# Performance work log

Hardware: AMD Instinct MI355X
Metric: run time of the kernel (lower is better)

The kernel has to match this reference:

```python
import jax, jax.numpy as jnp
import numpy as np

N = 65536          # nodes
G = 512            # graphs (num_segments for scatter-mean)
NB = 10            # number_of_basis
MAXR = 10.0        # max_radius
NODE_DIM = 64      # 48 z-embed + 16 mol-embed scalars
MUL = 16           # multiplicity of each output irrep l=0..3
WNUM = NODE_DIM * 4 * MUL  # tp weight numel = 4096
MID = 32           # middle_layer_size

_trapz = getattr(np, 'trapezoid', np.trapz)

def _silu_norm():
    # e3nn normalize2mom constant for silu: 1/sqrt(E_{z~N(0,1)}[silu(z)^2]) ~= 1.679
    z = np.linspace(-12.0, 12.0, 200001)
    pdf = np.exp(-0.5 * z * z) / np.sqrt(2.0 * np.pi)
    s = z / (1.0 + np.exp(-z))
    return float(_trapz(s * s * pdf, z) ** -0.5)

SILU_C = _silu_norm()

def soft_unit_step(x):
    pos = x > 0
    return jnp.where(pos, jnp.exp(-1.0 / jnp.where(pos, x, 1.0)), 0.0)

def soft_one_hot_smooth_finite(x):
    # e3nn soft_one_hot_linspace(basis='smooth_finite', cutoff=True)
    values = jnp.linspace(0.0, MAXR, NB + 2)[1:-1]
    step = MAXR / (NB + 1)
    diff = (x[:, None] - values) / step
    c = 1.14136 * float(np.exp(2.0))
    return c * soft_unit_step(diff + 1.0) * soft_unit_step(1.0 - diff)

def spherical_harmonics_lmax3(vec):
    # e3nn convention, normalize=True, normalization='component' (each l scaled by sqrt(2l+1))
    u = vec / jnp.linalg.norm(vec, axis=-1, keepdims=True)
    x, y, z = u[..., 0], u[..., 1], u[..., 2]
    s3 = np.sqrt(3.0)
    y2, x2z2 = y * y, x * x + z * z
    sh0 = jnp.ones_like(x)[..., None]
    s20 = s3 * x * z; s21 = s3 * x * y; s22 = y2 - 0.5 * x2z2
    s23 = s3 * y * z; s24 = 0.5 * s3 * (z * z - x * x)
    s30 = np.sqrt(5.0 / 6.0) * (s20 * z + s24 * x)
    s31 = np.sqrt(5.0) * s20 * y
    s32 = np.sqrt(3.0 / 8.0) * (4.0 * y2 - x2z2) * x
    s33 = 0.5 * y * (2.0 * y2 - 3.0 * x2z2)
    s34 = np.sqrt(3.0 / 8.0) * z * (4.0 * y2 - x2z2)
    s35 = np.sqrt(5.0) * s24 * y
    s36 = np.sqrt(5.0 / 6.0) * (s24 * z - s20 * x)
    sh1 = np.sqrt(3.0) * jnp.stack([x, y, z], -1)
    sh2 = np.sqrt(5.0) * jnp.stack([s20, s21, s22, s23, s24], -1)
    sh3 = np.sqrt(7.0) * jnp.stack([s30, s31, s32, s33, s34, s35, s36], -1)
    return (sh0, sh1, sh2, sh3)

def setup_inputs() -> dict:
    key = jax.random.key(0)
    ks = jax.random.split(key, 8)
    pos = 3.0 * jax.random.normal(ks[0], (N, 3), jnp.float32)
    x = jax.random.randint(ks[1], (N,), 0, 100)
    mol_id = jax.random.randint(ks[2], (N,), 0, 3)
    batch = jnp.sort(jax.random.randint(ks[3], (N,), 0, G))
    emb_z = jax.random.normal(ks[4], (100, 48), jnp.float32)
    emb_mol = jax.random.normal(ks[5], (3, 16), jnp.float32)
    W1 = jax.random.normal(ks[6], (NB, MID), jnp.float32)
    W2 = jax.random.normal(ks[7], (MID, WNUM), jnp.float32)
    return {'pos': pos, 'x': x, 'mol_id': mol_id, 'batch': batch,
            'emb_z': emb_z, 'emb_mol': emb_mol, 'W1': W1, 'W2': W2}

def reference(pos, x, mol_id, batch, emb_z, emb_mol, W1, W2):
    feat = jnp.concatenate([emb_z[x], emb_mol[mol_id]], axis=-1)        # [N, 64]
    length = jnp.linalg.norm(pos, axis=1)
    basis = soft_one_hot_smooth_finite(length) * np.sqrt(float(NB))     # [N, 10]
    # e3nn FullyConnectedNet([10, 32, 4096], silu): weight / sqrt(fan_in), normalized silu
    h = SILU_C * jax.nn.silu(basis @ (W1 / np.sqrt(float(NB))))         # [N, 32]
    w = h @ (W2 / np.sqrt(float(MID)))                                  # [N, 4096]
    # path weight sqrt((2l+1)/64) times w3j(0,l,l)=I/sqrt(2l+1) -> net factor 1/sqrt(64)
    w = w.reshape(-1, 4, NODE_DIM, MUL)
    xw = jnp.einsum('eu,eluw->elw', feat, w) / np.sqrt(float(NODE_DIM))  # [N, 4, 16]
    shs = spherical_harmonics_lmax3(pos)
    blocks = [(xw[:, l, :, None] * shs[l][:, None, :]).reshape(-1, MUL * (2 * l + 1)) for l in range(4)]
    value = jnp.concatenate(blocks, axis=-1)                            # [N, 256]
    sums = jax.ops.segment_sum(value, batch, num_segments=G)
    counts = jax.ops.segment_sum(jnp.ones((value.shape[0], 1), value.dtype), batch, num_segments=G)
    return sums / jnp.maximum(counts, 1.0)                              # scatter-mean [G, 256]
```

## Files before the change

kernel.cpp:

```cpp
#include <hip/hip_runtime.h>
#include <math.h>

#define N_NODES 65536
#define G_SEG   512
#define NE      256

#define NB_HS 33
#define NB_Q  128
#define NB_QM 32
#define NB_S  3
#define NB_P0 (N_NODES / 256)
#define NB_K1 (NB_HS + NB_Q + NB_QM + NB_S + NB_P0)

#define NB_A  1700
#define NB_B2 257
#define NB_K2 (NB_A + NB_B2)

#define A_ELEMS  (257 * 100 * 64)
#define B_ELEMS  (257 * 3 * 64)
#define Q_ELEMS  (100 * 32 * 64)
#define QM_ELEMS (3 * 32 * 64)
#define HS_ELEMS (257 * 32)

__global__ __launch_bounds__(256) void prep1(
    const float* __restrict__ emb_z, const float* __restrict__ emb_mol,
    const float* __restrict__ W2, const float* __restrict__ W1,
    const int* __restrict__ batch,
    const float* __restrict__ pos, const int* __restrict__ xz,
    const int* __restrict__ mol,
    float* __restrict__ Q, float* __restrict__ Qm, float* __restrict__ hs,
    int* __restrict__ seg, float4* __restrict__ aux, float silu_c)
{
    __shared__ float w2s[64 * 49];
    __shared__ float ezq[1200];

    const int b = blockIdx.x;
    const int t = threadIdx.x;

    if (b < NB_HS) {
        const int tid = b * 256 + t;
        if (tid >= HS_ELEMS) return;
        const int e = tid >> 5, m = tid & 31;
        const float L = (float)e * (10.f / (float)NE);
        const float c = 8.4335412f;
        float p = 0.f;
#pragma unroll
        for (int k = 0; k < 10; ++k) {
            const float a  = 1.1f * L - (float)k;
            const float bb = (float)(k + 2) - 1.1f * L;
            const float bas = (a > 0.f && bb > 0.f) ? c * __expf(-2.f / (a * bb)) : 0.f;
            p = fmaf(bas, W1[k * 32 + m], p);
        }
        const float scale = 0.02209708691207961f;
        hs[tid] = scale * silu_c * p / (1.f + __expf(-p));
    } else if (b < NB_HS + NB_Q) {
        const int q  = b - NB_HS;
        const int m  = q >> 2;
        const int zq = q & 3;
        for (int p = t; p < 3072; p += 256) {
            const int l = p / 768, r = p - l * 768;
            w2s[((l * 16) + (r & 15)) * 49 + (r >> 4)] = W2[m * 4096 + l * 1024 + r];
        }
        for (int p = t; p < 1200; p += 256) ezq[p] = emb_z[zq * 1200 + p];
        __syncthreads();

        const int zg = t >> 6, cc = t & 63;
#pragma unroll
        for (int zi = 0; zi < 7; ++zi) {
            const int zl = zg + 4 * zi;
            if (zl < 25) {
                float a0 = 0.f, a1 = 0.f, a2 = 0.f, a3 = 0.f;
#pragma unroll
                for (int u = 0; u < 48; u += 4) {
                    a0 = fmaf(ezq[zl * 48 + u + 0], w2s[cc * 49 + u + 0], a0);
                    a1 = fmaf(ezq[zl * 48 + u + 1], w2s[cc * 49 + u + 1], a1);
                    a2 = fmaf(ezq[zl * 48 + u + 2], w2s[cc * 49 + u + 2], a2);
                    a3 = fmaf(ezq[zl * 48 + u + 3], w2s[cc * 49 + u + 3], a3);
                }
                Q[(((zq * 25 + zl) * 32 + m) << 6) + cc] = (a0 + a1) + (a2 + a3);
            }
        }
    } else if (b < NB_HS + NB_Q + NB_QM) {
        const int m = b - (NB_HS + NB_Q);
        if (t < 192) {
            const int mo = t >> 6, j = t & 63;
            const float* wp = W2 + m * 4096 + (j >> 4) * 1024 + 768 + (j & 15);
            float acc = 0.f;
#pragma unroll
            for (int v = 0; v < 16; ++v)
                acc = fmaf(emb_mol[mo * 16 + v], wp[v * 16], acc);
            Qm[((mo * 32 + m) << 6) + j] = acc;
        }
    } else if (b < NB_HS + NB_Q + NB_QM + NB_S) {
        const int g = (b - NB_HS - NB_Q - NB_QM) * 256 + t;
        if (g > G_SEG) return;
        int lo = 0, hi = N_NODES;
        while (lo < hi) {
            const int mid = (lo + hi) >> 1;
            if (batch[mid] < g) lo = mid + 1; else hi = mid;
        }
        seg[g] = lo;
    } else {
        const int i = (b - NB_HS - NB_Q - NB_QM - NB_S) * 256 + t;
        const float px = pos[3 * i], py = pos[3 * i + 1], pz = pos[3 * i + 2];
        const int z  = xz[i];
        const int mo = mol[i];
        const float Lsq = px * px + py * py + pz * pz;
        const float rinv = __builtin_amdgcn_rsqf(Lsq);
        const float L = Lsq * rinv;
        const float tt = fminf(L * ((float)NE / 10.0f), 255.999f);
        const int e = (int)tt;
        const int fr15 = min((int)((tt - (float)e) * 32768.f), 32767);
        float4 a;
        a.x = px * rinv; a.y = py * rinv; a.z = pz * rinv;
        a.w = __uint_as_float(((unsigned)e << 24) | ((unsigned)z << 17) |
                              ((unsigned)mo << 15) | (unsigned)fr15);
        aux[i] = a;
    }
}

__global__ __launch_bounds__(256) void build_AB2(
    const float* __restrict__ Q, const float* __restrict__ Qm,
    const float* __restrict__ hs,
    float* __restrict__ A, float* __restrict__ B)
{
    const int b = blockIdx.x;
    const int t = threadIdx.x;
    const int j = t & 63;
    const int er = __builtin_amdgcn_readfirstlane(t >> 6);

    if (b < NB_A) {
        const int et = b / 100;
        const int z  = b - et * 100;
        float Qr[32];
        const float* Qp = Q + ((z * 32) << 6) + j;
#pragma unroll
        for (int m = 0; m < 32; ++m) Qr[m] = Qp[m << 6];

        const int e0 = et * 16;
#pragma unroll
        for (int p4 = 0; p4 < 4; ++p4) {
            const int e = e0 + er + 4 * p4;
            if (e < 257) {
                const float* hp = hs + e * 32;
                float a0 = 0.f, a1 = 0.f, a2 = 0.f, a3 = 0.f;
#pragma unroll
                for (int m = 0; m < 32; m += 4) {
                    a0 = fmaf(hp[m + 0], Qr[m + 0], a0);
                    a1 = fmaf(hp[m + 1], Qr[m + 1], a1);
                    a2 = fmaf(hp[m + 2], Qr[m + 2], a2);
                    a3 = fmaf(hp[m + 3], Qr[m + 3], a3);
                }
                A[((e * 100 + z) << 6) + j] = (a0 + a1) + (a2 + a3);
            }
        }
    } else {
        const int e  = b - NB_A;
        const int mo = t >> 6;
        if (mo < 3) {
            const float* Qp = Qm + ((mo * 32) << 6) + j;
            const float* hp = hs + e * 32;
            float acc = 0.f;
#pragma unroll
            for (int m = 0; m < 32; ++m)
                acc = fmaf(hp[m], Qp[m << 6], acc);
            B[((e * 3 + mo) << 6) + j] = acc;
        }
    }
}

__global__ __launch_bounds__(1024) void seg_mean(
    const float4* __restrict__ aux, const int* __restrict__ seg,
    const float* __restrict__ A, const float* __restrict__ B,
    float* __restrict__ out)
{
    __shared__ float red[16 * 257];

    const int g  = blockIdx.x;
    const int s0 = seg[g], s1 = seg[g + 1];
    const int cnt = s1 - s0;

    const int w16  = __builtin_amdgcn_readfirstlane(threadIdx.x >> 6);
    const int l    = w16 & 3;
    const int qt   = w16 >> 2;
    const int lane = threadIdx.x & 63;
    const int ns   = lane >> 4;
    const int wi   = lane & 15;
    const int jj   = l * 16 + wi;

    const int q0 = s0 + ((cnt * qt) >> 2);
    const int q1 = s0 + ((cnt * (qt + 1)) >> 2);

    float acc[7];
#pragma unroll
    for (int k = 0; k < 7; ++k) acc[k] = 0.f;

    const int niter = (q1 - q0 + 3) >> 2;

    float4 aN = make_float4(0.f, 0.f, 1.f, __uint_as_float(0u));
    float a0N = 0.f, a1N = 0.f, b0N = 0.f, b1N = 0.f;
    if (niter > 0) {
        const int ic = min(q0 + ns, q1 - 1);
        aN = aux[ic];
        const unsigned cd = __float_as_uint(aN.w);
        const float* Ar = A + (((cd >> 24) * 100 + ((cd >> 17) & 127u)) << 6) + jj;
        const float* Br = B + (((cd >> 24) * 3 + ((cd >> 15) & 3u)) << 6) + jj;
        a0N = Ar[0]; a1N = Ar[6400]; b0N = Br[0]; b1N = Br[192];
    }

    for (int it = 0; it < niter; ++it) {
        const float4 a = aN;
        const float f0 = a0N + b0N, f1 = a1N + b1N;
        const unsigned code = __float_as_uint(a.w);
        const int i = q0 + it * 4 + ns;
        const bool valid = (i < q1);

        if (it + 1 < niter) {
            const int ic = min(q0 + (it + 1) * 4 + ns, q1 - 1);
            aN = aux[ic];
            const unsigned cn = __float_as_uint(aN.w);
            const float* Ar = A + (((cn >> 24) * 100 + ((cn >> 17) & 127u)) << 6) + jj;
            const float* Br = B + (((cn >> 24) * 3 + ((cn >> 15) & 3u)) << 6) + jj;
            a0N = Ar[0]; a1N = Ar[6400]; b0N = Br[0]; b1N = Br[192];
        }

        const float fr = (float)(code & 32767u) * 3.0517578125e-5f;
        float xwv = fmaf(fr, f1 - f0, f0);
        xwv = valid ? xwv : 0.f;

        const float ux = a.x, uy = a.y, uz = a.z;
        const float s3 = 1.7320508075688772f, s5 = 2.2360679774997896f, s7 = 2.6457513110645907f;

        if (l == 0) {
            acc[0] += xwv;
        } else if (l == 1) {
            acc[0] = fmaf(xwv, s3 * ux, acc[0]);
            acc[1] = fmaf(xwv, s3 * uy, acc[1]);
            acc[2] = fmaf(xwv, s3 * uz, acc[2]);
        } else if (l == 2) {
            const float y2 = uy * uy, x2z2 = ux * ux + uz * uz;
            const float s20 = s3 * ux * uz;
            const float s21 = s3 * ux * uy;
            const float s22 = y2 - 0.5f * x2z2;
            const float s23 = s3 * uy * uz;
            const float s24 = 0.5f * s3 * (uz * uz - ux * ux);
            const float xs = xwv * s5;
            acc[0] = fmaf(xs, s20, acc[0]);
            acc[1] = fmaf(xs, s21, acc[1]);
            acc[2] = fmaf(xs, s22, acc[2]);
            acc[3] = fmaf(xs, s23, acc[3]);
            acc[4] = fmaf(xs, s24, acc[4]);
        } else {
            const float y2 = uy * uy, x2z2 = ux * ux + uz * uz;
            const float s20 = s3 * ux * uz;
            const float s24 = 0.5f * s3 * (uz * uz - ux * ux);
            const float c56 = 0.9128709291752769f;
            const float c38 = 0.6123724356957945f;
            const float r4 = 4.f * y2 - x2z2;
            const float s30 = c56 * (s20 * uz + s24 * ux);
            const float s31 = s5 * s20 * uy;
            const float s32 = c38 * r4 * ux;
            const float s33 = 0.5f * uy * (2.f * y2 - 3.f * x2z2);
            const float s34 = c38 * uz * r4;
            const float s35 = s5 * s24 * uy;
            const float s36 = c56 * (s24 * uz - s20 * ux);
            const float xs = xwv * s7;
            acc[0] = fmaf(xs, s30, acc[0]);
            acc[1] = fmaf(xs, s31, acc[1]);
            acc[2] = fmaf(xs, s32, acc[2]);
            acc[3] = fmaf(xs, s33, acc[3]);
            acc[4] = fmaf(xs, s34, acc[4]);
            acc[5] = fmaf(xs, s35, acc[5]);
            acc[6] = fmaf(xs, s36, acc[6]);
        }
    }

    const int nl = 2 * l + 1;
    const int off = (l == 0 ? 0 : (l == 1 ? 16 : (l == 2 ? 64 : 144)));
    const int base = off + wi * nl;
#pragma unroll
    for (int k = 0; k < 7; ++k)
        if (k < nl) red[(qt * 4 + ns) * 257 + base + k] = acc[k];
    __syncthreads();

    if (threadIdx.x < 256) {
        float s = 0.f;
#pragma unroll
        for (int ww = 0; ww < 16; ++ww) s += red[ww * 257 + threadIdx.x];
        out[g * 256 + threadIdx.x] = s / (float)max(cnt, 1);
    }
}

static double silu_c_host()
{
    const int n = 200001;
    const double h = 24.0 / 200000.0;
    double sum = 0.0, prev = 0.0;
    for (int i = 0; i < n; ++i) {
        const double z = -12.0 + h * (double)i;
        const double pdf = exp(-0.5 * z * z) * 0.3989422804014327;
        const double s = z / (1.0 + exp(-z));
        const double f = s * s * pdf;
        if (i) sum += prev + f;
        prev = f;
    }
    sum *= 0.5 * h;
    return 1.0 / sqrt(sum);
}

extern "C" void kernel_launch(void* const* d_in, const int* in_sizes, int n_in,
                              void* d_out, int out_size, void* d_ws, size_t ws_size,
                              hipStream_t stream)
{
    const float* pos     = (const float*)d_in[0];
    const int*   xz      = (const int*)d_in[1];
    const int*   mol     = (const int*)d_in[2];
    const int*   batch   = (const int*)d_in[3];
    const float* emb_z   = (const float*)d_in[4];
    const float* emb_mol = (const float*)d_in[5];
    const float* W1      = (const float*)d_in[6];
    const float* W2      = (const float*)d_in[7];
    float* out = (float*)d_out;

    float4* aux  = (float4*)d_ws;
    float*  Abuf = (float*)d_ws + 4 * N_NODES;
    float*  Bbuf = Abuf + A_ELEMS;
    float*  Qbuf = Bbuf + B_ELEMS;
    float*  Qmb  = Qbuf + Q_ELEMS;
    float*  hsb  = Qmb + QM_ELEMS;
    int*    seg  = (int*)(hsb + HS_ELEMS);

    static const float SILU_C_F = (float)silu_c_host();

    prep1<<<NB_K1, 256, 0, stream>>>(emb_z, emb_mol, W2, W1, batch,
                                     pos, xz, mol, Qbuf, Qmb, hsb, seg, aux, SILU_C_F);
    build_AB2<<<NB_K2, 256, 0, stream>>>(Qbuf, Qmb, hsb, Abuf, Bbuf);
    seg_mean<<<G_SEG, 1024, 0, stream>>>(aux, seg, Abuf, Bbuf, out);
}
```

Before: 33.72 us.

## Interleave adjacent radial table entries as float2 and deepen aux prefetch

```diff
diff --git a/kernel.cpp b/kernel.cpp
--- a/kernel.cpp
+++ b/kernel.cpp
@@ -16,8 +16,8 @@
 #define NB_B2 257
 #define NB_K2 (NB_A + NB_B2)
 
-#define A_ELEMS  (257 * 100 * 64)
-#define B_ELEMS  (257 * 3 * 64)
+#define AP_ELEMS (256 * 100 * 128)
+#define BP_ELEMS (256 * 3 * 128)
 #define Q_ELEMS  (100 * 32 * 64)
 #define QM_ELEMS (3 * 32 * 64)
 #define HS_ELEMS (257 * 32)
@@ -122,7 +122,7 @@
 __global__ __launch_bounds__(256) void build_AB2(
     const float* __restrict__ Q, const float* __restrict__ Qm,
     const float* __restrict__ hs,
-    float* __restrict__ A, float* __restrict__ B)
+    float* __restrict__ AP, float* __restrict__ BP)
 {
     const int b = blockIdx.x;
     const int t = threadIdx.x;
@@ -151,7 +151,9 @@
                     a2 = fmaf(hp[m + 2], Qr[m + 2], a2);
                     a3 = fmaf(hp[m + 3], Qr[m + 3], a3);
                 }
-                A[((e * 100 + z) << 6) + j] = (a0 + a1) + (a2 + a3);
+                const float v = (a0 + a1) + (a2 + a3);
+                if (e < 256) AP[((e * 100 + z) << 7) + 2 * j] = v;
+                if (e > 0)   AP[(((e - 1) * 100 + z) << 7) + 2 * j + 1] = v;
             }
         }
     } else {
@@ -164,14 +166,15 @@
 #pragma unroll
             for (int m = 0; m < 32; ++m)
                 acc = fmaf(hp[m], Qp[m << 6], acc);
-            B[((e * 3 + mo) << 6) + j] = acc;
+            if (e < 256) BP[((e * 3 + mo) << 7) + 2 * j] = acc;
+            if (e > 0)   BP[(((e - 1) * 3 + mo) << 7) + 2 * j + 1] = acc;
         }
     }
 }
 
 __global__ __launch_bounds__(1024) void seg_mean(
     const float4* __restrict__ aux, const int* __restrict__ seg,
-    const float* __restrict__ A, const float* __restrict__ B,
+    const float2* __restrict__ AP2, const float2* __restrict__ BP2,
     float* __restrict__ out)
 {
     __shared__ float red[16 * 257];
@@ -197,38 +200,38 @@
 
     const int niter = (q1 - q0 + 3) >> 2;
 
-    float4 aN = make_float4(0.f, 0.f, 1.f, __uint_as_float(0u));
-    float a0N = 0.f, a1N = 0.f, b0N = 0.f, b1N = 0.f;
+    float4 axC = make_float4(0.f, 0.f, 1.f, __uint_as_float(0u));
+    float4 axN = axC;
+    float2 avC = make_float2(0.f, 0.f), bvC = avC;
+
+    if (niter > 0) axC = aux[min(q0 + ns, q1 - 1)];
+    if (niter > 1) axN = aux[min(q0 + 4 + ns, q1 - 1)];
     if (niter > 0) {
-        const int ic = min(q0 + ns, q1 - 1);
-        aN = aux[ic];
-        const unsigned cd = __float_as_uint(aN.w);
-        const float* Ar = A + (((cd >> 24) * 100 + ((cd >> 17) & 127u)) << 6) + jj;
-        const float* Br = B + (((cd >> 24) * 3 + ((cd >> 15) & 3u)) << 6) + jj;
-        a0N = Ar[0]; a1N = Ar[6400]; b0N = Br[0]; b1N = Br[192];
+        const unsigned cd = __float_as_uint(axC.w);
+        avC = AP2[((cd >> 24) * 100 + ((cd >> 17) & 127u)) * 64 + jj];
+        bvC = BP2[((cd >> 24) * 3 + ((cd >> 15) & 3u)) * 64 + jj];
     }
 
     for (int it = 0; it < niter; ++it) {
-        const float4 a = aN;
-        const float f0 = a0N + b0N, f1 = a1N + b1N;
-        const unsigned code = __float_as_uint(a.w);
+        float2 avN = avC, bvN = bvC;
+        float4 axNN = axN;
+        if (it + 1 < niter) {
+            const unsigned cn = __float_as_uint(axN.w);
+            avN = AP2[((cn >> 24) * 100 + ((cn >> 17) & 127u)) * 64 + jj];
+            bvN = BP2[((cn >> 24) * 3 + ((cn >> 15) & 3u)) * 64 + jj];
+        }
+        if (it + 2 < niter)
+            axNN = aux[min(q0 + (it + 2) * 4 + ns, q1 - 1)];
+
+        const unsigned code = __float_as_uint(axC.w);
         const int i = q0 + it * 4 + ns;
         const bool valid = (i < q1);
-
-        if (it + 1 < niter) {
-            const int ic = min(q0 + (it + 1) * 4 + ns, q1 - 1);
-            aN = aux[ic];
-            const unsigned cn = __float_as_uint(aN.w);
-            const float* Ar = A + (((cn >> 24) * 100 + ((cn >> 17) & 127u)) << 6) + jj;
-            const float* Br = B + (((cn >> 24) * 3 + ((cn >> 15) & 3u)) << 6) + jj;
-            a0N = Ar[0]; a1N = Ar[6400]; b0N = Br[0]; b1N = Br[192];
-        }
-
         const float fr = (float)(code & 32767u) * 3.0517578125e-5f;
+        const float f0 = avC.x + bvC.x, f1 = avC.y + bvC.y;
         float xwv = fmaf(fr, f1 - f0, f0);
         xwv = valid ? xwv : 0.f;
 
-        const float ux = a.x, uy = a.y, uz = a.z;
+        const float ux = axC.x, uy = axC.y, uz = axC.z;
         const float s3 = 1.7320508075688772f, s5 = 2.2360679774997896f, s7 = 2.6457513110645907f;
 
         if (l == 0) {
@@ -273,6 +276,8 @@
             acc[5] = fmaf(xs, s35, acc[5]);
             acc[6] = fmaf(xs, s36, acc[6]);
         }
+
+        axC = axN; axN = axNN; avC = avN; bvC = bvN;
     }
 
     const int nl = 2 * l + 1;
@@ -323,9 +328,9 @@
     float* out = (float*)d_out;
 
     float4* aux  = (float4*)d_ws;
-    float*  Abuf = (float*)d_ws + 4 * N_NODES;
-    float*  Bbuf = Abuf + A_ELEMS;
-    float*  Qbuf = Bbuf + B_ELEMS;
+    float*  APb  = (float*)d_ws + 4 * N_NODES;
+    float*  BPb  = APb + AP_ELEMS;
+    float*  Qbuf = BPb + BP_ELEMS;
     float*  Qmb  = Qbuf + Q_ELEMS;
     float*  hsb  = Qmb + QM_ELEMS;
     int*    seg  = (int*)(hsb + HS_ELEMS);
@@ -334,6 +339,7 @@
 
     prep1<<<NB_K1, 256, 0, stream>>>(emb_z, emb_mol, W2, W1, batch,
                                      pos, xz, mol, Qbuf, Qmb, hsb, seg, aux, SILU_C_F);
-    build_AB2<<<NB_K2, 256, 0, stream>>>(Qbuf, Qmb, hsb, Abuf, Bbuf);
-    seg_mean<<<G_SEG, 1024, 0, stream>>>(aux, seg, Abuf, Bbuf, out);
-}
+    build_AB2<<<NB_K2, 256, 0, stream>>>(Qbuf, Qmb, hsb, APb, BPb);
+    seg_mean<<<G_SEG, 1024, 0, stream>>>(aux, seg, (const float2*)APb,
+                                         (const float2*)BPb, out);
+}
```

After: 37.14 us. +10.1%, slower.
